# Kernel tuning notes

Hardware: AMD Instinct MI355X
Metric: run time of the kernel (lower is better)

## Reference

```python
import jax, jax.numpy as jnp
import numpy as np

IN_DIM = 4096
OUT_DIM = 4096
RANK = 64
MULTIPLIER = 1.0
SCALE = 1.0  # alpha / lora_dim = 64 / 64


def setup_inputs() -> dict:
    key = jax.random.key(0)
    ks = jax.random.split(key, 8)
    x = jax.random.normal(ks[0], (4, 4096, IN_DIM), dtype=jnp.float32)
    # frozen original module weight (Linear, no bias): [out, in]
    W_org = jax.random.normal(ks[1], (OUT_DIM, IN_DIM), dtype=jnp.float32) * 0.02
    # trainable adapter: q (down) [r, in], p (up) [out, r], lambda [1, r]
    q_w = jax.random.normal(ks[2], (RANK, IN_DIM), dtype=jnp.float32) * 0.02
    p_w = jax.random.normal(ks[3], (OUT_DIM, RANK), dtype=jnp.float32) * 0.02
    lam = jnp.abs(jax.random.normal(ks[4], (1, RANK), dtype=jnp.float32)) / np.sqrt(RANK)
    # frozen base copies (deepcopied at init; here distinct values to exercise the subtraction)
    base_q_w = jax.random.normal(ks[5], (RANK, IN_DIM), dtype=jnp.float32) * 0.02
    base_p_w = jax.random.normal(ks[6], (OUT_DIM, RANK), dtype=jnp.float32) * 0.02
    base_lam = jnp.abs(jax.random.normal(ks[7], (1, RANK), dtype=jnp.float32)) / np.sqrt(RANK)
    return {"x": x, "W_org": W_org, "q_w": q_w, "p_w": p_w, "lam": lam,
            "base_q_w": base_q_w, "base_p_w": base_p_w, "base_lam": base_lam}


def reference(x, W_org, q_w, p_w, lam, base_q_w, base_p_w, base_lam):
    # original module forward (Linear, no bias)
    org = jnp.einsum('bsd,od->bso', x, W_org)
    # adapter path: P((Q x) * lambda)
    lx = jnp.einsum('bsr,or->bso', jnp.einsum('bsd,rd->bsr', x, q_w) * lam, p_w)
    # frozen base path: base_P((base_Q x) * base_lambda)
    base_lx = jnp.einsum('bsr,or->bso', jnp.einsum('bsd,rd->bsr', x, base_q_w) * base_lam, base_p_w)
    return org + (lx - base_lx) * (MULTIPLIER * SCALE)
```

## Files before the change

kernel.cpp:

```cpp
#include <hip/hip_runtime.h>
#include <hip/hip_bf16.h>

typedef __hip_bfloat16 bf16;
typedef __attribute__((ext_vector_type(8))) short short8;
typedef __attribute__((ext_vector_type(4))) float floatx4;

#define K_DIM 4096
#define N_DIM 4096
#define M_DIM 16384
#define RANK  64

__global__ __launch_bounds__(256) void cvt_x_kernel(
    const float4* __restrict__ in, short8* __restrict__ out)
{
    const int i = blockIdx.x * 256 + threadIdx.x;
    const float4 a = in[2 * i];
    const float4 b = in[2 * i + 1];
    bf16 t[8];
    t[0] = __float2bfloat16(a.x); t[1] = __float2bfloat16(a.y);
    t[2] = __float2bfloat16(a.z); t[3] = __float2bfloat16(a.w);
    t[4] = __float2bfloat16(b.x); t[5] = __float2bfloat16(b.y);
    t[6] = __float2bfloat16(b.z); t[7] = __float2bfloat16(b.w);
    out[i] = *(const short8*)t;
}

__global__ __launch_bounds__(256) void prep_weff_kernel(
    const float* __restrict__ W, const float* __restrict__ q,
    const float* __restrict__ p, const float* __restrict__ lam,
    const float* __restrict__ bq, const float* __restrict__ bp,
    const float* __restrict__ blam, bf16* __restrict__ Weff)
{
    const int k  = blockIdx.x * 256 + threadIdx.x;
    const int n0 = blockIdx.y * 8;
    float acc[8];
#pragma unroll
    for (int i = 0; i < 8; ++i) acc[i] = 0.0f;

    for (int r = 0; r < RANK; ++r) {
        const float qlv  = lam[r]  * q [r * K_DIM + k];
        const float bqlv = blam[r] * bq[r * K_DIM + k];
#pragma unroll
        for (int i = 0; i < 8; ++i) {
            acc[i] += p [(n0 + i) * RANK + r] * qlv;
            acc[i] -= bp[(n0 + i) * RANK + r] * bqlv;
        }
    }
#pragma unroll
    for (int i = 0; i < 8; ++i) {
        const size_t idx = (size_t)(n0 + i) * K_DIM + k;
        Weff[idx] = __float2bfloat16(W[idx] + acc[i]);
    }
}

__device__ __forceinline__ void stage2(const bf16* g0, const bf16* g1, char* d)
{
    __builtin_amdgcn_global_load_lds(
        (const __attribute__((address_space(1))) void*)g0,
        (__attribute__((address_space(3))) void*)d, 16, 0, 0);
    __builtin_amdgcn_global_load_lds(
        (const __attribute__((address_space(1))) void*)g1,
        (__attribute__((address_space(3))) void*)(d + 8192), 16, 0, 0);
}

__device__ __forceinline__ void lda4(short8 (&dst)[4], const char* base,
                                     int off, int kb)
{
#pragma unroll
    for (int fr = 0; fr < 4; ++fr)
        dst[fr] = *(const short8*)(base + off + fr * 2048 + kb);
}

__device__ __forceinline__ void ldb4(short8 (&dst)[4], const char* base,
                                     int off, int kb)
{
#pragma unroll
    for (int fc = 0; fc < 4; ++fc)
        dst[fc] = *(const short8*)(base + off + fc * 2048 + kb);
}

__device__ __forceinline__ void mma16(floatx4 (&acc)[8][4], int rbase,
                                      const short8 (&av)[4], const short8 (&bv)[4])
{
#pragma unroll
    for (int fr = 0; fr < 4; ++fr)
#pragma unroll
        for (int fc = 0; fc < 4; ++fc)
            acc[rbase + fr][fc] = __builtin_amdgcn_mfma_f32_16x16x32_bf16(
                av[fr], bv[fc], acc[rbase + fr][fc], 0, 0, 0);
}

#define PHASE_TAIL(LG_, R0_, AV_, BV_) do {                    \
    __builtin_amdgcn_s_barrier();                              \
    asm volatile("s_waitcnt lgkmcnt(" #LG_ ")" ::: "memory");  \
    __builtin_amdgcn_s_setprio(1);                             \
    mma16(acc, R0_, AV_, BV_);                                 \
    __builtin_amdgcn_s_setprio(0);                             \
    __builtin_amdgcn_s_barrier();                              \
} while (0)

#define PHASE_TAIL_VM(R0_, AV_, BV_) do {                      \
    __builtin_amdgcn_s_barrier();                              \
    asm volatile("s_waitcnt lgkmcnt(0)" ::: "memory");         \
    __builtin_amdgcn_s_setprio(1);                             \
    mma16(acc, R0_, AV_, BV_);                                 \
    __builtin_amdgcn_s_setprio(0);                             \
    asm volatile("s_waitcnt vmcnt(8)" ::: "memory");           \
    __builtin_amdgcn_s_barrier();                              \
} while (0)

__global__ __launch_bounds__(512, 2) void gemm256_8ph_kernel(
    const bf16* __restrict__ A, const bf16* __restrict__ B, float* __restrict__ C)
{
    __shared__ __align__(16) char lds_buf[163840];

    const int tid  = threadIdx.x;
    const int lane = tid & 63;
    const int wave = tid >> 6;
    const int wm   = wave >> 2;
    const int wn   = wave & 3;

    const int bid = blockIdx.x;
    const int wg  = (bid & 7) * 128 + (bid >> 3);
    const int bx  = wg & 15;
    const int by  = wg >> 4;
    const int tm  = by * 256;
    const int tn  = bx * 256;

    const int r0  = tid >> 3;
    const int csw = (((tid & 7) ^ (r0 & 7)) << 3);
    const bf16* gA0 = A + (size_t)(tm +       r0) * K_DIM + csw;
    const bf16* gA1 = A + (size_t)(tm +  64 + r0) * K_DIM + csw;
    const bf16* gA2 = A + (size_t)(tm + 128 + r0) * K_DIM + csw;
    const bf16* gA3 = A + (size_t)(tm + 192 + r0) * K_DIM + csw;
    const bf16* gB0 = B + (size_t)(tn +       r0) * K_DIM + csw;
    const bf16* gB1 = B + (size_t)(tn +  64 + r0) * K_DIM + csw;
    const bf16* gB2 = B + (size_t)(tn + 128 + r0) * K_DIM + csw;
    const bf16* gB3 = B + (size_t)(tn + 192 + r0) * K_DIM + csw;

    char* ldsA = (char*)lds_buf;
    char* ldsB = ldsA + 65536;
    const int wb = wave * 1024;

    const int l15 = lane & 15;
    const int kb0 = ((lane >> 4) << 4) ^ ((lane & 7) << 4);
    const int kb1 = kb0 ^ 64;
    const char* aB = ldsA + (wm * 128 + l15) * 128;
    const char* bB = ldsB + (wn * 64  + l15) * 128;

    floatx4 acc[8][4];
#pragma unroll
    for (int p = 0; p < 8; ++p)
#pragma unroll
        for (int q = 0; q < 4; ++q) acc[p][q] = (floatx4){0.f, 0.f, 0.f, 0.f};

    short8 a0k0[4], a0k1[4], a1k0[4], a1k1[4], bk0[4], bk1[4];

    stage2(gA0, gA1, ldsA + wb);
    stage2(gA2, gA3, ldsA + 16384 + wb);
    stage2(gA0 + 64, gA1 + 64, ldsA + 32768 + wb);
    stage2(gA2 + 64, gA3 + 64, ldsA + 32768 + 16384 + wb);
    stage2(gB0, gB1, ldsB + wb);
    stage2(gB2, gB3, ldsB + 16384 + wb);
    stage2(gB0 + 64, gB1 + 64, ldsB + 32768 + wb);
    stage2(gB2 + 64, gB3 + 64, ldsB + 32768 + 16384 + wb);
    asm volatile("s_waitcnt vmcnt(0)" ::: "memory");
    __builtin_amdgcn_s_barrier();

    int bO0 = 0, bO1 = 32768, bO2 = 65536;

#pragma unroll 1
    for (int i = 0; i < 32; ++i) {
        const int kt2 = ((2 * i + 2 < 64) ? (2 * i + 2) : 63) * 64;
        const int kt3 = ((2 * i + 3 < 64) ? (2 * i + 3) : 63) * 64;

        lda4(a0k0, aB, 0, kb0);
        ldb4(bk0, bB, bO0, kb0);
        lda4(a0k1, aB, 0, kb1);
        stage2(gB0 + kt2, gB1 + kt2, ldsB + bO2 + wb);
        PHASE_TAIL(4, 0, a0k0, bk0);

        lda4(a1k0, aB, 8192, kb0);
        lda4(a1k1, aB, 8192, kb1);
        stage2(gB2 + kt2, gB3 + kt2, ldsB + bO2 + 16384 + wb);
        PHASE_TAIL(4, 4, a1k0, bk0);

        ldb4(bk1, bB, bO0, kb1);
        stage2(gA0 + kt2, gA1 + kt2, ldsA + wb);
        PHASE_TAIL(0, 0, a0k1, bk1);

        stage2(gA2 + kt2, gA3 + kt2, ldsA + 16384 + wb);
        PHASE_TAIL_VM(4, a1k1, bk1);

        lda4(a0k0, aB, 32768, kb0);
        ldb4(bk0, bB, bO1, kb0);
        lda4(a0k1, aB, 32768, kb1);
        stage2(gB0 + kt3, gB1 + kt3, ldsB + bO0 + wb);
        PHASE_TAIL(4, 0, a0k0, bk0);

        lda4(a1k0, aB, 32768 + 8192, kb0);
        lda4(a1k1, aB, 32768 + 8192, kb1);
        stage2(gB2 + kt3, gB3 + kt3, ldsB + bO0 + 16384 + wb);
        PHASE_TAIL(4, 4, a1k0, bk0);

        ldb4(bk1, bB, bO1, kb1);
        stage2(gA0 + kt3, gA1 + kt3, ldsA + 32768 + wb);
        PHASE_TAIL(0, 0, a0k1, bk1);

        stage2(gA2 + kt3, gA3 + kt3, ldsA + 32768 + 16384 + wb);
        PHASE_TAIL_VM(4, a1k1, bk1);

        const int tmp = bO2; bO2 = bO1; bO1 = bO0; bO0 = tmp;
    }

    const int row0 = tm + wm * 128 + (lane >> 4) * 4;
    const int col0 = tn + wn * 64 + l15;
#pragma unroll
    for (int mf = 0; mf < 8; ++mf)
#pragma unroll
        for (int fc = 0; fc < 4; ++fc)
#pragma unroll
            for (int rr = 0; rr < 4; ++rr)
                C[(size_t)(row0 + mf * 16 + rr) * N_DIM + (col0 + fc * 16)] =
                    acc[mf][fc][rr];
}

extern "C" void kernel_launch(void* const* d_in, const int* in_sizes, int n_in,
                              void* d_out, int out_size, void* d_ws, size_t ws_size,
                              hipStream_t stream)
{
    const float* x    = (const float*)d_in[0];
    const float* Worg = (const float*)d_in[1];
    const float* qw   = (const float*)d_in[2];
    const float* pw   = (const float*)d_in[3];
    const float* lam  = (const float*)d_in[4];
    const float* bqw  = (const float*)d_in[5];
    const float* bpw  = (const float*)d_in[6];
    const float* blam = (const float*)d_in[7];
    float* out = (float*)d_out;

    bf16* x_bf = (bf16*)d_ws;
    bf16* Weff = (bf16*)((char*)d_ws + (size_t)M_DIM * K_DIM * 2);

    cvt_x_kernel<<<dim3((M_DIM * K_DIM) / (8 * 256)), 256, 0, stream>>>(
        (const float4*)x, (short8*)x_bf);

    prep_weff_kernel<<<dim3(K_DIM / 256, N_DIM / 8), 256, 0, stream>>>(
        Worg, qw, pw, lam, bqw, bpw, blam, Weff);

    gemm256_8ph_kernel<<<dim3(1024), 512, 0, stream>>>(x_bf, Weff, out);
}
```

Before: 1.053 ms.

## Restructure GEMM main loop to double-buffered 8-phase schedule with smaller LDS

Replaces the triple-buffered B ring (160 KB LDS) with a fixed double-buffered A/B layout (128 KB) and reorders the eight phases. LDS fragments for the next phase are now prefetched one phase ahead, and global stages are interleaved per half-tile. Wait counts change to lgkmcnt(8)/vmcnt(4) so more loads stay in flight. The smaller LDS footprint may ease occupancy, but the tighter buffer reuse increases the risk of hazards if the wait counts are off.

```diff
diff --git a/kernel.cpp b/kernel.cpp
--- a/kernel.cpp
+++ b/kernel.cpp
@@ -89,7 +89,7 @@
                 av[fr], bv[fc], acc[rbase + fr][fc], 0, 0, 0);
 }
 
-#define PHASE_TAIL(LG_, R0_, AV_, BV_) do {                    \
+#define TAIL(LG_, R0_, AV_, BV_) do {                          \
     __builtin_amdgcn_s_barrier();                              \
     asm volatile("s_waitcnt lgkmcnt(" #LG_ ")" ::: "memory");  \
     __builtin_amdgcn_s_setprio(1);                             \
@@ -98,20 +98,20 @@
     __builtin_amdgcn_s_barrier();                              \
 } while (0)
 
-#define PHASE_TAIL_VM(R0_, AV_, BV_) do {                      \
-    __builtin_amdgcn_s_barrier();                              \
-    asm volatile("s_waitcnt lgkmcnt(0)" ::: "memory");         \
+#define TAIL_VM(LG_, R0_, AV_, BV_) do {                       \
+    __builtin_amdgcn_s_barrier();                              \
+    asm volatile("s_waitcnt lgkmcnt(" #LG_ ")" ::: "memory");  \
     __builtin_amdgcn_s_setprio(1);                             \
     mma16(acc, R0_, AV_, BV_);                                 \
     __builtin_amdgcn_s_setprio(0);                             \
-    asm volatile("s_waitcnt vmcnt(8)" ::: "memory");           \
+    asm volatile("s_waitcnt vmcnt(4)" ::: "memory");           \
     __builtin_amdgcn_s_barrier();                              \
 } while (0)
 
 __global__ __launch_bounds__(512, 2) void gemm256_8ph_kernel(
     const bf16* __restrict__ A, const bf16* __restrict__ B, float* __restrict__ C)
 {
-    __shared__ __align__(16) char lds_buf[163840];
+    __shared__ __align__(16) char lds_buf[131072];
 
     const int tid  = threadIdx.x;
     const int lane = tid & 63;
@@ -144,8 +144,8 @@
     const int l15 = lane & 15;
     const int kb0 = ((lane >> 4) << 4) ^ ((lane & 7) << 4);
     const int kb1 = kb0 ^ 64;
-    const char* aB = ldsA + (wm * 128 + l15) * 128;
-    const char* bB = ldsB + (wn * 64  + l15) * 128;
+    const char* aB = ldsA + wm * 16384 + l15 * 128;
+    const char* bB = ldsB + wn * 8192  + l15 * 128;
 
     floatx4 acc[8][4];
 #pragma unroll
@@ -153,63 +153,61 @@
 #pragma unroll
         for (int q = 0; q < 4; ++q) acc[p][q] = (floatx4){0.f, 0.f, 0.f, 0.f};
 
-    short8 a0k0[4], a0k1[4], a1k0[4], a1k1[4], bk0[4], bk1[4];
+    short8 a0k0[4], a1k0[4], a0k1[4], a1k1[4], bk0[4], bk1[4];
 
     stage2(gA0, gA1, ldsA + wb);
     stage2(gA2, gA3, ldsA + 16384 + wb);
-    stage2(gA0 + 64, gA1 + 64, ldsA + 32768 + wb);
-    stage2(gA2 + 64, gA3 + 64, ldsA + 32768 + 16384 + wb);
     stage2(gB0, gB1, ldsB + wb);
     stage2(gB2, gB3, ldsB + 16384 + wb);
+    stage2(gA0 + 64, gA1 + 64, ldsA + 32768 + wb);
     stage2(gB0 + 64, gB1 + 64, ldsB + 32768 + wb);
-    stage2(gB2 + 64, gB3 + 64, ldsB + 32768 + 16384 + wb);
-    asm volatile("s_waitcnt vmcnt(0)" ::: "memory");
+    stage2(gB2 + 64, gB3 + 64, ldsB + 49152 + wb);
+    asm volatile("s_waitcnt vmcnt(6)" ::: "memory");
     __builtin_amdgcn_s_barrier();
-
-    int bO0 = 0, bO1 = 32768, bO2 = 65536;
+    lda4(a0k0, aB, 0, kb0);
+    ldb4(bk0, bB, 0, kb0);
 
 #pragma unroll 1
     for (int i = 0; i < 32; ++i) {
+        const int kt1 = (2 * i + 1) * 64;
         const int kt2 = ((2 * i + 2 < 64) ? (2 * i + 2) : 63) * 64;
         const int kt3 = ((2 * i + 3 < 64) ? (2 * i + 3) : 63) * 64;
 
+        lda4(a1k0, aB, 8192, kb0);
+        lda4(a0k1, aB, 0, kb1);
+        stage2(gA2 + kt1, gA3 + kt1, ldsA + 49152 + wb);
+        TAIL(8, 0, a0k0, bk0);
+
+        ldb4(bk1, bB, 0, kb1);
+        lda4(a1k1, aB, 8192, kb1);
+        stage2(gA0 + kt2, gA1 + kt2, ldsA + wb);
+        TAIL_VM(8, 4, a1k0, bk0);
+
+        lda4(a0k0, aB, 32768, kb0);
+        ldb4(bk0, bB, 32768, kb0);
+        stage2(gA2 + kt2, gA3 + kt2, ldsA + 16384 + wb);
+        TAIL_VM(8, 0, a0k1, bk1);
+
+        lda4(a1k0, aB, 32768 + 8192, kb0);
+        lda4(a0k1, aB, 32768, kb1);
+        stage2(gB0 + kt2, gB1 + kt2, ldsB + wb);
+        TAIL(8, 4, a1k1, bk1);
+
+        ldb4(bk1, bB, 32768, kb1);
+        lda4(a1k1, aB, 32768 + 8192, kb1);
+        stage2(gB2 + kt2, gB3 + kt2, ldsB + 16384 + wb);
+        TAIL(8, 0, a0k0, bk0);
+
+        stage2(gB0 + kt3, gB1 + kt3, ldsB + 32768 + wb);
+        TAIL(8, 4, a1k0, bk0);
+
+        stage2(gB2 + kt3, gB3 + kt3, ldsB + 49152 + wb);
+        TAIL_VM(0, 0, a0k1, bk1);
+
         lda4(a0k0, aB, 0, kb0);
-        ldb4(bk0, bB, bO0, kb0);
-        lda4(a0k1, aB, 0, kb1);
-        stage2(gB0 + kt2, gB1 + kt2, ldsB + bO2 + wb);
-        PHASE_TAIL(4, 0, a0k0, bk0);
-
-        lda4(a1k0, aB, 8192, kb0);
-        lda4(a1k1, aB, 8192, kb1);
-        stage2(gB2 + kt2, gB3 + kt2, ldsB + bO2 + 16384 + wb);
-        PHASE_TAIL(4, 4, a1k0, bk0);
-
-        ldb4(bk1, bB, bO0, kb1);
-        stage2(gA0 + kt2, gA1 + kt2, ldsA + wb);
-        PHASE_TAIL(0, 0, a0k1, bk1);
-
-        stage2(gA2 + kt2, gA3 + kt2, ldsA + 16384 + wb);
-        PHASE_TAIL_VM(4, a1k1, bk1);
-
-        lda4(a0k0, aB, 32768, kb0);
-        ldb4(bk0, bB, bO1, kb0);
-        lda4(a0k1, aB, 32768, kb1);
-        stage2(gB0 + kt3, gB1 + kt3, ldsB + bO0 + wb);
-        PHASE_TAIL(4, 0, a0k0, bk0);
-
-        lda4(a1k0, aB, 32768 + 8192, kb0);
-        lda4(a1k1, aB, 32768 + 8192, kb1);
-        stage2(gB2 + kt3, gB3 + kt3, ldsB + bO0 + 16384 + wb);
-        PHASE_TAIL(4, 4, a1k0, bk0);
-
-        ldb4(bk1, bB, bO1, kb1);
+        ldb4(bk0, bB, 0, kb0);
         stage2(gA0 + kt3, gA1 + kt3, ldsA + 32768 + wb);
-        PHASE_TAIL(0, 0, a0k1, bk1);
-
-        stage2(gA2 + kt3, gA3 + kt3, ldsA + 32768 + 16384 + wb);
-        PHASE_TAIL_VM(4, a1k1, bk1);
-
-        const int tmp = bO2; bO2 = bO1; bO1 = bO0; bO0 = tmp;
+        TAIL(8, 4, a1k1, bk1);
     }
 
     const int row0 = tm + wm * 128 + (lane >> 4) * 4;
```

Measured after the change: 1.582 ms. 1.5x slower.
